# Kernel optimization log

Hardware: AMD Instinct MI355X
Metric: run time of the kernel (lower is better)

The kernel has to match this reference:

```python
import jax, jax.numpy as jnp
import numpy as np

B, S, E = 2, 4096, 2560
H, HKV, D = 8, 4, 256
WINDOW = 1024
SOFTCAP = 50.0
SCALING = 256.0 ** -0.5  # query_pre_attn_scalar = 256
EPS = 1e-6
MASK_VAL = -2.3819763e38


def rms_norm(x, w):
    # RMSNorm with add_unit_offset=True, computed in float32
    xf = x.astype(jnp.float32)
    out = xf * jax.lax.rsqrt(jnp.mean(xf * xf, axis=-1, keepdims=True) + EPS)
    return (out * (1.0 + w.astype(jnp.float32))).astype(x.dtype)


def apply_rotary_emb(x, cos, sin):
    # x: [B, S, h, D]; cos/sin: [S, D/2]; half-split rotation
    x1, x2 = jnp.split(x, 2, axis=-1)
    c = cos[None, :, None, :]
    s = sin[None, :, None, :]
    return jnp.concatenate([x1 * c - x2 * s, x2 * c + x1 * s], axis=-1)


def setup_inputs() -> dict:
    key = jax.random.key(0)
    ks = jax.random.split(key, 6)
    hidden_states = jax.random.normal(ks[0], (B, S, E), dtype=jnp.float32)
    # RoPE frequencies, theta=10000
    inv_freq = 1.0 / (10000.0 ** (np.arange(0, D, 2, dtype=np.float32) / D))
    t = np.arange(S, dtype=np.float32)
    freqs = np.outer(t, inv_freq)  # [S, D/2]
    freqs_cos = jnp.asarray(np.cos(freqs), dtype=jnp.float32)
    freqs_sin = jnp.asarray(np.sin(freqs), dtype=jnp.float32)
    kv_write_indices = jnp.arange(S, dtype=jnp.int32)
    k_cache = jnp.zeros((B, S, HKV, D), dtype=jnp.float32)
    v_cache = jnp.zeros((B, S, HKV, D), dtype=jnp.float32)
    # causal mask and causal+sliding-window mask (additive)
    i = np.arange(S)[:, None]
    j = np.arange(S)[None, :]
    causal = j <= i
    sliding = causal & ((i - j) < WINDOW)
    mask = jnp.asarray(np.where(causal, 0.0, MASK_VAL), dtype=jnp.float32)
    mask = jnp.broadcast_to(mask[None, None], (B, 1, S, S))
    local_mask = jnp.asarray(np.where(sliding, 0.0, MASK_VAL), dtype=jnp.float32)
    local_mask = jnp.broadcast_to(local_mask[None, None], (B, 1, S, S))
    w_qkv = jax.random.normal(ks[1], ((H + 2 * HKV) * D, E), dtype=jnp.float32) * (E ** -0.5)
    w_o = jax.random.normal(ks[2], (E, H * D), dtype=jnp.float32) * ((H * D) ** -0.5)
    q_norm_w = jnp.zeros((D,), dtype=jnp.float32)
    k_norm_w = jnp.zeros((D,), dtype=jnp.float32)
    return dict(hidden_states=hidden_states, freqs_cos=freqs_cos, freqs_sin=freqs_sin,
                kv_write_indices=kv_write_indices, k_cache=k_cache, v_cache=v_cache,
                mask=mask, local_mask=local_mask, w_qkv=w_qkv, w_o=w_o,
                q_norm_w=q_norm_w, k_norm_w=k_norm_w)


def reference(hidden_states, freqs_cos, freqs_sin, kv_write_indices, k_cache, v_cache,
              mask, local_mask, w_qkv, w_o, q_norm_w, k_norm_w):
    bsz, input_len, _ = hidden_states.shape
    qkv = jnp.einsum('bse,fe->bsf', hidden_states, w_qkv)
    xq, xk, xv = jnp.split(qkv, [H * D, H * D + HKV * D], axis=-1)
    xq = xq.reshape(bsz, input_len, H, D)
    xk = xk.reshape(bsz, input_len, HKV, D)
    xv = xv.reshape(bsz, input_len, HKV, D)
    # QK RMSNorm
    xq = rms_norm(xq, q_norm_w)
    xk = rms_norm(xk, k_norm_w)
    # RoPE
    xq = apply_rotary_emb(xq, freqs_cos, freqs_sin)
    xk = apply_rotary_emb(xk, freqs_cos, freqs_sin)
    # KV cache write
    k_cache = k_cache.at[:, kv_write_indices].set(xk)
    v_cache = v_cache.at[:, kv_write_indices].set(xv)
    kv_len = k_cache.shape[1]
    # GQA expand: [B, T, HKV, D] -> [B, T, H, D]
    nrep = H // HKV
    key = jnp.repeat(k_cache, nrep, axis=2)
    value = jnp.repeat(v_cache, nrep, axis=2)
    q = jnp.transpose(xq, (0, 2, 1, 3)) * SCALING   # [B, H, S, D]
    k = jnp.transpose(key, (0, 2, 1, 3))            # [B, H, T, D]
    v = jnp.transpose(value, (0, 2, 1, 3))
    scores = jnp.einsum('bhqd,bhkd->bhqk', q, k)
    # logit softcapping
    scores = jnp.tanh(scores / SOFTCAP) * SOFTCAP
    # attn_type == LOCAL_SLIDING -> use local (sliding-window) mask
    scores = scores + local_mask
    probs = jax.nn.softmax(scores.astype(jnp.float32), axis=-1).astype(q.dtype)
    out = jnp.einsum('bhqk,bhkd->bhqd', probs, v)
    out = jnp.transpose(out, (0, 2, 1, 3)).reshape(bsz, input_len, H * D)
    return jnp.einsum('bsf,ef->bse', out, w_o)
```

## Files before the change

### kernel.cpp

```cpp
#include <hip/hip_runtime.h>
#include <stdint.h>
#include <stddef.h>

#define B_    2
#define S_    4096
#define E_    2560
#define H_    8
#define HKV_  4
#define D_    256
#define F_    4096
#define HD_   2048
#define WIN_  1024
#define MASKNEG (-3.0e38f)

typedef __bf16 bf16;
typedef bf16  bf16x8 __attribute__((ext_vector_type(8)));
typedef bf16  bf16x4 __attribute__((ext_vector_type(4)));
typedef float f32x4  __attribute__((ext_vector_type(4)));
typedef uint32_t u32;

__device__ __forceinline__ void gl_lds16(const void* g, void* l) {
  __builtin_amdgcn_global_load_lds((const __attribute__((address_space(1))) void*)g,
                                   (__attribute__((address_space(3))) void*)l, 16, 0, 0);
}

__device__ __forceinline__ void bar_mf() {
  asm volatile("" ::: "memory");
  __builtin_amdgcn_s_barrier();
  asm volatile("" ::: "memory");
}

__device__ __forceinline__ float softcap50(float x) {
  float t = x * 0.02f;
  t = fminf(fmaxf(t, -15.f), 15.f);
  float e = __expf(2.f * t);
  return 50.f * ((e - 1.f) / (e + 1.f));
}

__device__ __forceinline__ u32 pkbf16(float a, float b) {
  union { bf16 h[2]; u32 u; } cv;
  cv.h[0] = (bf16)a; cv.h[1] = (bf16)b; return cv.u;
}

__global__ __launch_bounds__(256) void to_bf16_plain(const float* __restrict__ src,
                                                     bf16* __restrict__ dst, int n) {
  const int i = (blockIdx.x * 256 + threadIdx.x) * 8;
  if (i >= n) return;
  f32x4 a = *(const f32x4*)(src + i);
  f32x4 b = *(const f32x4*)(src + i + 4);
  bf16x8 o;
#pragma unroll
  for (int j = 0; j < 4; ++j) { o[j] = (bf16)a[j]; o[j + 4] = (bf16)b[j]; }
  *(bf16x8*)(dst + i) = o;
}

template <int EPI>
__global__ __launch_bounds__(512, 2) void gemm_8ph(
    const bf16* __restrict__ A, const bf16* __restrict__ Bw, int Kd, int NT,
    bf16* __restrict__ qo, bf16* __restrict__ ko, bf16* __restrict__ vto,
    float* __restrict__ C, int Nout, int row_base) {
  __shared__ bf16 Lds[2][4][128 * 64];

  const int tid  = threadIdx.x;
  const int lane = tid & 63;
  const int wave = tid >> 6;
  const int wm   = wave >> 2;
  const int wn   = wave & 3;
  const int l16  = lane & 15;
  const int quad = lane >> 4;

  const int nwg  = gridDim.x * gridDim.y;
  const int obid = blockIdx.y * gridDim.x + blockIdx.x;
  const int bid  = (obid & 7) * (nwg >> 3) + (obid >> 3);
  const int mt   = bid / gridDim.x;
  const int ntl  = bid - mt * gridDim.x;
  const int row0 = mt * 256, col0 = ntl * 256;

  const bf16* Ah[2] = {A  + (size_t)row0 * Kd, A  + (size_t)(row0 + 128) * Kd};
  const bf16* Bh[2] = {Bw + (size_t)col0 * Kd, Bw + (size_t)(col0 + 128) * Kd};

  auto stage = [&](int dbf, int hf, const bf16* src, int k0) {
#pragma unroll
    for (int i = 0; i < 2; ++i) {
      const int g = tid + i * 512;
      const int r = g >> 3, c = g & 7;
      gl_lds16(src + (size_t)r * Kd + k0 + ((c ^ (r & 7)) << 3),
               &Lds[dbf][hf][0] + g * 8);
    }
  };
  auto rdA = [&](int dbf, int i, int ks) -> bf16x8 {
    const int r = i * 16 + l16;
    return *(const bf16x8*)&Lds[dbf][wm][r * 64 + (((ks * 4 + quad) ^ (r & 7)) << 3)];
  };
  auto rdB = [&](int dbf, int j, int ks) -> bf16x8 {
    const int r = (wn & 1) * 64 + j * 16 + l16;
    return *(const bf16x8*)&Lds[dbf][2 + (wn >> 1)][r * 64 + (((ks * 4 + quad) ^ (r & 7)) << 3)];
  };

  f32x4 acc[8][4] = {};

  stage(0, 0, Ah[0], 0); stage(0, 1, Ah[1], 0);
  stage(0, 2, Bh[0], 0); stage(0, 3, Bh[1], 0);
  if (NT > 1) { stage(1, 2, Bh[0], 64); stage(1, 3, Bh[1], 64); }
  asm volatile("s_waitcnt vmcnt(4)" ::: "memory");
  bar_mf();

  int db = 0;
  for (int t = 0; t < NT; ++t, db ^= 1) {
    const int k1 = (t + 1) * 64, k2 = (t + 2) * 64;
    const bool st1 = (t + 1 < NT), st2 = (t + 2 < NT);

    bf16x8 bfr[4][2], a[4][2], a2[4][2];
#pragma unroll
    for (int j = 0; j < 4; ++j) { bfr[j][0] = rdB(db, j, 0); bfr[j][1] = rdB(db, j, 1); }
#pragma unroll
    for (int i = 0; i < 4; ++i) { a[i][0] = rdA(db, i, 0); a[i][1] = rdA(db, i, 1); }
    if (st1) stage(db ^ 1, 0, Ah[0], k1);
    bar_mf();
    __builtin_amdgcn_s_setprio(1);
#pragma unroll
    for (int i = 0; i < 2; ++i)
#pragma unroll
      for (int j = 0; j < 4; ++j) {
        acc[i][j] = __builtin_amdgcn_mfma_f32_16x16x32_bf16(a[i][0], bfr[j][0], acc[i][j], 0, 0, 0);
        acc[i][j] = __builtin_amdgcn_mfma_f32_16x16x32_bf16(a[i][1], bfr[j][1], acc[i][j], 0, 0, 0);
      }
    __builtin_amdgcn_s_setprio(0);
    bar_mf();

#pragma unroll
    for (int i = 0; i < 4; ++i) { a2[i][0] = rdA(db, i + 4, 0); a2[i][1] = rdA(db, i + 4, 1); }
    if (st1) stage(db ^ 1, 1, Ah[1], k1);
    bar_mf();
    __builtin_amdgcn_s_setprio(1);
#pragma unroll
    for (int i = 2; i < 4; ++i)
#pragma unroll
      for (int j = 0; j < 4; ++j) {
        acc[i][j] = __builtin_amdgcn_mfma_f32_16x16x32_bf16(a[i][0], bfr[j][0], acc[i][j], 0, 0, 0);
        acc[i][j] = __builtin_amdgcn_mfma_f32_16x16x32_bf16(a[i][1], bfr[j][1], acc[i][j], 0, 0, 0);
      }
    __builtin_amdgcn_s_setprio(0);
    bar_mf();

    if (st2) stage(db, 2, Bh[0], k2);
    bar_mf();
    __builtin_amdgcn_s_setprio(1);
#pragma unroll
    for (int i = 0; i < 2; ++i)
#pragma unroll
      for (int j = 0; j < 4; ++j) {
        acc[i + 4][j] = __builtin_amdgcn_mfma_f32_16x16x32_bf16(a2[i][0], bfr[j][0], acc[i + 4][j], 0, 0, 0);
        acc[i + 4][j] = __builtin_amdgcn_mfma_f32_16x16x32_bf16(a2[i][1], bfr[j][1], acc[i + 4][j], 0, 0, 0);
      }
    __builtin_amdgcn_s_setprio(0);
    bar_mf();

    if (st2) stage(db, 3, Bh[1], k2);
    bar_mf();
    __builtin_amdgcn_s_setprio(1);
#pragma unroll
    for (int i = 2; i < 4; ++i)
#pragma unroll
      for (int j = 0; j < 4; ++j) {
        acc[i + 4][j] = __builtin_amdgcn_mfma_f32_16x16x32_bf16(a2[i][0], bfr[j][0], acc[i + 4][j], 0, 0, 0);
        acc[i + 4][j] = __builtin_amdgcn_mfma_f32_16x16x32_bf16(a2[i][1], bfr[j][1], acc[i + 4][j], 0, 0, 0);
      }
    __builtin_amdgcn_s_setprio(0);
    if (st2) asm volatile("s_waitcnt vmcnt(4)" ::: "memory");
    else     asm volatile("s_waitcnt vmcnt(0)" ::: "memory");
    bar_mf();
  }

#pragma unroll
  for (int i = 0; i < 8; ++i) {
    const int rbase = row_base + row0 + wm * 128 + i * 16 + quad * 4;
#pragma unroll
    for (int j = 0; j < 4; ++j) {
      const int c = col0 + wn * 64 + j * 16 + l16;
      if constexpr (EPI == 1) {
        int head = c >> 8;
        const int d = c & 255;
        if (head < 12) {
          bf16* base; int nh;
          if (head < 8) { base = qo; nh = H_; }
          else          { base = ko; nh = HKV_; head -= 8; }
#pragma unroll
          for (int rr = 0; rr < 4; ++rr) {
            const int row = rbase + rr;
            const int bb = row >> 12, s = row & 4095;
            base[(((size_t)(bb * nh + head) * S_) + s) * D_ + d] = (bf16)acc[i][j][rr];
          }
        } else {
          const int kh = head - 12;
          const int bb = rbase >> 12, s0 = rbase & 4095;
          bf16x4 pk;
#pragma unroll
          for (int rr = 0; rr < 4; ++rr) pk[rr] = (bf16)acc[i][j][rr];
          *(bf16x4*)(vto + (((size_t)(bb * HKV_ + kh) * D_ + d) * S_ + s0)) = pk;
        }
      } else {
#pragma unroll
        for (int rr = 0; rr < 4; ++rr)
          C[(size_t)(rbase + rr) * Nout + c] = acc[i][j][rr];
      }
    }
  }
}

__global__ __launch_bounds__(192) void normrope2(
    bf16* __restrict__ q, bf16* __restrict__ k,
    const float* __restrict__ fcos, const float* __restrict__ fsin,
    const int* __restrict__ widx,
    const float* __restrict__ qnw, const float* __restrict__ knw) {
  const int bx  = blockIdx.x;
  const int b   = bx >> 12;
  const int s   = bx & 4095;
  const int tid = threadIdx.x;
  const int hh  = tid >> 4;
  const int g   = tid & 15;
  const int d0  = g * 16;

  const bool isq = (hh < 8);
  bf16* rowp = isq ? (q + (((size_t)(b * H_ + hh) * S_ + s) * D_ + d0))
                   : (k + (((size_t)(b * HKV_ + (hh - 8)) * S_ + s) * D_ + d0));
  float x[16];
  {
    bf16x8 v0 = *(const bf16x8*)rowp;
    bf16x8 v1 = *(const bf16x8*)(rowp + 8);
#pragma unroll
    for (int i = 0; i < 8; ++i) { x[i] = (float)v0[i]; x[i + 8] = (float)v1[i]; }
  }

  float ssq = 0.f;
#pragma unroll
  for (int i = 0; i < 16; ++i) ssq += x[i] * x[i];
#pragma unroll
  for (int off = 1; off < 16; off <<= 1) ssq += __shfl_xor(ssq, off);
  const float sc = rsqrtf(ssq * (1.0f / 256.0f) + 1e-6f);
  const float* w = isq ? qnw : knw;
#pragma unroll
  for (int i = 0; i < 16; ++i) x[i] = x[i] * sc * (1.0f + w[d0 + i]);

  const int fbase = (g < 8) ? d0 : (d0 - 128);
  const float* cp = fcos + (size_t)s * 128 + fbase;
  const float* sp = fsin + (size_t)s * 128 + fbase;
#pragma unroll
  for (int i = 0; i < 16; ++i) {
    const float c = cp[i], sn = sp[i];
    const float other = __shfl_xor(x[i], 8);
    x[i] = (g < 8) ? (x[i] * c - other * sn)
                   : (x[i] * c + other * sn);
  }
  if (isq) {
#pragma unroll
    for (int i = 0; i < 16; ++i) x[i] *= 0.0625f;
  }

  bf16x8 o0, o1;
#pragma unroll
  for (int i = 0; i < 8; ++i) { o0[i] = (bf16)x[i]; o1[i] = (bf16)x[i + 8]; }

  bf16* dstp = isq ? rowp
                   : (k + (((size_t)(b * HKV_ + (hh - 8)) * S_ + widx[s]) * D_ + d0));
  *(bf16x8*)dstp = o0;
  *(bf16x8*)(dstp + 8) = o1;
}

__global__ __launch_bounds__(256) void attn_mfma(const bf16* __restrict__ Q,
                                                 const bf16* __restrict__ K,
                                                 const bf16* __restrict__ Vt,
                                                 bf16* __restrict__ out) {
  __shared__ bf16 Ks[2][32 * 256];
  __shared__ bf16 Vs[2][256 * 32];

  const int hw  = blockIdx.x;
  const int lid = (hw & 7) * 128 + (hw >> 3);
  const int bx  = lid & 63;
  const int bh  = lid >> 6;
  const int b   = bh >> 3, h = bh & 7, kh = h >> 1;

  const int lane = threadIdx.x & 63;
  const int wave = threadIdx.x >> 6;
  const int l16  = lane & 15;
  const int qd   = lane >> 4;
  const int swz  = l16 & 7;

  const int q0w = bx * 64 + wave * 16;
  const int iq  = q0w + l16;

  const bf16* Kb = K  + ((size_t)(b * HKV_ + kh) * S_) * D_;
  const bf16* Vb = Vt + ((size_t)(b * HKV_ + kh) * D_) * S_;

  bf16x8 qf[8];
  {
    const bf16* qp = Q + (((size_t)(b * H_ + h) * S_ + iq) * D_) + qd * 8;
#pragma unroll
    for (int kc = 0; kc < 8; ++kc) qf[kc] = *(const bf16x8*)(qp + kc * 32);
  }

  f32x4 Od[16] = {};
  float m = MASKNEG, l = 0.f;

  int lo = bx * 64 - (WIN_ - 1); if (lo < 0) lo = 0;
  lo &= ~31;
  const int t1 = bx * 64 + 32;

  auto stage = [&](int buf, int kt) {
#pragma unroll
    for (int i = 0; i < 4; ++i) {
      const int r0  = wave * 8 + i * 2;
      const int row = r0 + (lane >> 5);
      const int c   = lane & 31;
      gl_lds16(Kb + (size_t)(kt + row) * D_ + ((c ^ (row & 7)) * 8),
               &Ks[buf][r0 * 256] + lane * 8);
    }
#pragma unroll
    for (int i = 0; i < 4; ++i) {
      const int d0 = (wave * 4 + i) * 16;
      const int d  = d0 + (lane >> 2);
      gl_lds16(Vb + (size_t)d * S_ + kt + (lane & 3) * 8,
               &Vs[buf][d0 * 32] + lane * 8);
    }
  };

  stage(0, lo);
  int buf = 0;

  for (int kt = lo; kt <= t1; kt += 32) {
    const bool pre = (kt + 32 <= t1);
    if (pre) {
      stage(buf ^ 1, kt + 32);
      asm volatile("s_waitcnt vmcnt(8)" ::: "memory");
    } else {
      asm volatile("s_waitcnt vmcnt(0)" ::: "memory");
    }
    __builtin_amdgcn_s_barrier();
    asm volatile("" ::: "memory");

    const bool dead = (kt > q0w + 15) || (kt + 31 < q0w - (WIN_ - 1));
    if (!dead) {
      f32x4 sacc[2] = {};
#pragma unroll
      for (int kc = 0; kc < 8; ++kc) {
        const int ch = ((kc * 4 + qd) ^ swz) * 8;
        bf16x8 k0 = *(const bf16x8*)&Ks[buf][l16 * 256 + ch];
        bf16x8 k1 = *(const bf16x8*)&Ks[buf][(l16 + 16) * 256 + ch];
        sacc[0] = __builtin_amdgcn_mfma_f32_16x16x32_bf16(k0, qf[kc], sacc[0], 0, 0, 0);
        sacc[1] = __builtin_amdgcn_mfma_f32_16x16x32_bf16(k1, qf[kc], sacc[1], 0, 0, 0);
      }

      float scv[8];
#pragma unroll
      for (int t = 0; t < 2; ++t)
#pragma unroll
        for (int r = 0; r < 4; ++r) {
          const int jj = kt + t * 16 + qd * 4 + r;
          const float a = softcap50(sacc[t][r]);
          scv[t * 4 + r] = (jj <= iq && (iq - jj) < WIN_) ? a : MASKNEG;
        }

      float mx = scv[0];
#pragma unroll
      for (int i = 1; i < 8; ++i) mx = fmaxf(mx, scv[i]);
      mx = fmaxf(mx, __shfl_xor(mx, 16));
      mx = fmaxf(mx, __shfl_xor(mx, 32));
      const float mn = fmaxf(m, mx);
      const float alpha = __expf(m - mn);

      float p[8], ls = 0.f;
#pragma unroll
      for (int i = 0; i < 8; ++i) {
        p[i] = (scv[i] > -1e37f) ? __expf(scv[i] - mn) : 0.f;
        ls += p[i];
      }
      ls += __shfl_xor(ls, 16);
      ls += __shfl_xor(ls, 32);
      l = l * alpha + ls;
      m = mn;
#pragma unroll
      for (int dt = 0; dt < 16; ++dt) Od[dt] *= alpha;

      const u32 w0 = pkbf16(p[0], p[1]);
      const u32 w1 = pkbf16(p[2], p[3]);
      const u32 w2 = pkbf16(p[4], p[5]);
      const u32 w3 = pkbf16(p[6], p[7]);
      const int sA = l16 + ((2 * qd) & 3) * 16;
      const int sB = l16 + ((2 * qd + 1) & 3) * 16;
      const int a0 = __shfl((int)w0, sA), a1 = __shfl((int)w1, sA);
      const int a2 = __shfl((int)w2, sA), a3 = __shfl((int)w3, sA);
      const int b0 = __shfl((int)w0, sB), b1 = __shfl((int)w1, sB);
      const int b2 = __shfl((int)w2, sB), b3 = __shfl((int)w3, sB);
      const bool thi = (qd >> 1) != 0;
      union { int i4[4]; bf16x8 v; } pf;
      pf.i4[0] = thi ? a2 : a0;
      pf.i4[1] = thi ? a3 : a1;
      pf.i4[2] = thi ? b2 : b0;
      pf.i4[3] = thi ? b3 : b1;

#pragma unroll
      for (int dt = 0; dt < 16; ++dt) {
        bf16x8 vf = *(const bf16x8*)&Vs[buf][(dt * 16 + l16) * 32 + qd * 8];
        Od[dt] = __builtin_amdgcn_mfma_f32_16x16x32_bf16(vf, pf.v, Od[dt], 0, 0, 0);
      }
    }

    asm volatile("" ::: "memory");
    __builtin_amdgcn_s_barrier();
    buf ^= 1;
  }

  const float inv = 1.f / l;
  bf16* op = out + ((size_t)b * S_ + iq) * HD_ + h * D_ + qd * 4;
#pragma unroll
  for (int dt = 0; dt < 16; ++dt) {
    bf16x4 o4;
#pragma unroll
    for (int r = 0; r < 4; ++r) o4[r] = (bf16)(Od[dt][r] * inv);
    *(bf16x4*)(op + dt * 16) = o4;
  }
}

extern "C" void kernel_launch(void* const* d_in, const int* in_sizes, int n_in,
                              void* d_out, int out_size, void* d_ws, size_t ws_size,
                              hipStream_t stream) {
  const float* hidden = (const float*)d_in[0];
  const float* fcos   = (const float*)d_in[1];
  const float* fsin   = (const float*)d_in[2];
  const int*   widx   = (const int*)d_in[3];
  const float* wqkv   = (const float*)d_in[8];
  const float* wo     = (const float*)d_in[9];
  const float* qnw    = (const float*)d_in[10];
  const float* knw    = (const float*)d_in[11];
  float* out = (float*)d_out;

  char* ws = (char*)d_ws;
  const size_t MB = 1024 * 1024;
  const bool big = ws_size >= 126 * MB;

  bf16* wb_bf = (bf16*)(ws);
  bf16* hb_bf = (bf16*)(ws + 20 * MB);
  bf16* q_ws  = (bf16*)(ws + (big ? 60 : 32) * MB);
  bf16* k_ws  = (bf16*)(ws + (big ? 92 : 64) * MB);
  bf16* vt_ws = (bf16*)(ws + (big ? 108 : 80) * MB);
  bf16* att_o = (bf16*)(ws);
  bf16* wo_bf = (bf16*)(ws + 32 * MB);

  to_bf16_plain<<<(F_ * E_ / 8 + 255) / 256, 256, 0, stream>>>(wqkv, wb_bf, F_ * E_);

  const int nch   = big ? 1 : 4;
  const int chrow = (B_ * S_) / nch;
  for (int c = 0; c < nch; ++c) {
    const int row_base = c * chrow;
    to_bf16_plain<<<(chrow * E_ / 8 + 255) / 256, 256, 0, stream>>>(
        hidden + (size_t)row_base * E_, hb_bf, chrow * E_);
    gemm_8ph<1><<<dim3(F_ / 256, chrow / 256), 512, 0, stream>>>(
        hb_bf, wb_bf, E_, E_ / 64, q_ws, k_ws, vt_ws, nullptr, 0, row_base);
  }

  normrope2<<<dim3(B_ * S_), 192, 0, stream>>>(q_ws, k_ws, fcos, fsin, widx, qnw, knw);
  attn_mfma<<<dim3(1024), 256, 0, stream>>>(q_ws, k_ws, vt_ws, att_o);
  to_bf16_plain<<<(E_ * HD_ / 8 + 255) / 256, 256, 0, stream>>>(wo, wo_bf, E_ * HD_);
  gemm_8ph<0><<<dim3(E_ / 256, (B_ * S_) / 256), 512, 0, stream>>>(
      att_o, wo_bf, HD_, HD_ / 64, nullptr, nullptr, nullptr, out, E_, 0);
  (void)in_sizes; (void)n_in; (void)out_size;
}
```

Baseline: 858.3 us.

## Drop online-softmax max tracking using softcap bound, permute K rows, narrower GEMM tiles

The attention kernel drops running-max tracking and rescaling. Softcapped scores are bounded by 50, so exp(score-50) is computed directly through a sigmoid-style exp2 formulation, with masking skipped on interior tiles. K rows are permuted at load time so the P fragment can be packed without cross-lane shuffles. GEMMs gain a BN template parameter: the output projection and the small-workspace QKV path use 128-wide N tiles to put more workgroups on the grid. This relies on the softcap bound for numerical safety and adds a templated tile path.

```diff
diff --git a/kernel.cpp b/kernel.cpp
--- a/kernel.cpp
+++ b/kernel.cpp
@@ -11,7 +11,6 @@
 #define F_    4096
 #define HD_   2048
 #define WIN_  1024
-#define MASKNEG (-3.0e38f)
 
 typedef __bf16 bf16;
 typedef bf16  bf16x8 __attribute__((ext_vector_type(8)));
@@ -28,13 +27,6 @@
   asm volatile("" ::: "memory");
   __builtin_amdgcn_s_barrier();
   asm volatile("" ::: "memory");
-}
-
-__device__ __forceinline__ float softcap50(float x) {
-  float t = x * 0.02f;
-  t = fminf(fmaxf(t, -15.f), 15.f);
-  float e = __expf(2.f * t);
-  return 50.f * ((e - 1.f) / (e + 1.f));
 }
 
 __device__ __forceinline__ u32 pkbf16(float a, float b) {
@@ -54,12 +46,14 @@
   *(bf16x8*)(dst + i) = o;
 }
 
-template <int EPI>
+template <int EPI, int BN>
 __global__ __launch_bounds__(512, 2) void gemm_8ph(
     const bf16* __restrict__ A, const bf16* __restrict__ Bw, int Kd, int NT,
     bf16* __restrict__ qo, bf16* __restrict__ ko, bf16* __restrict__ vto,
     float* __restrict__ C, int Nout, int row_base) {
-  __shared__ bf16 Lds[2][4][128 * 64];
+  constexpr int NBH = BN / 128;
+  constexpr int JT  = BN / 64;
+  __shared__ bf16 Lds[2][2 + NBH][128 * 64];
 
   const int tid  = threadIdx.x;
   const int lane = tid & 63;
@@ -74,10 +68,11 @@
   const int bid  = (obid & 7) * (nwg >> 3) + (obid >> 3);
   const int mt   = bid / gridDim.x;
   const int ntl  = bid - mt * gridDim.x;
-  const int row0 = mt * 256, col0 = ntl * 256;
-
-  const bf16* Ah[2] = {A  + (size_t)row0 * Kd, A  + (size_t)(row0 + 128) * Kd};
-  const bf16* Bh[2] = {Bw + (size_t)col0 * Kd, Bw + (size_t)(col0 + 128) * Kd};
+  const int row0 = mt * 256, col0 = ntl * BN;
+
+  const bf16* Ah[2] = {A + (size_t)row0 * Kd, A + (size_t)(row0 + 128) * Kd};
+  const bf16* Bh[2] = {Bw + (size_t)col0 * Kd,
+                       Bw + (size_t)(col0 + (NBH == 2 ? 128 : 0)) * Kd};
 
   auto stage = [&](int dbf, int hf, const bf16* src, int k0) {
 #pragma unroll
@@ -93,16 +88,22 @@
     return *(const bf16x8*)&Lds[dbf][wm][r * 64 + (((ks * 4 + quad) ^ (r & 7)) << 3)];
   };
   auto rdB = [&](int dbf, int j, int ks) -> bf16x8 {
-    const int r = (wn & 1) * 64 + j * 16 + l16;
-    return *(const bf16x8*)&Lds[dbf][2 + (wn >> 1)][r * 64 + (((ks * 4 + quad) ^ (r & 7)) << 3)];
+    const int colt = wn * (BN / 4) + j * 16 + l16;
+    const int r = colt & 127;
+    return *(const bf16x8*)&Lds[dbf][2 + (colt >> 7)][r * 64 + (((ks * 4 + quad) ^ (r & 7)) << 3)];
   };
 
-  f32x4 acc[8][4] = {};
+  f32x4 acc[8][JT] = {};
 
   stage(0, 0, Ah[0], 0); stage(0, 1, Ah[1], 0);
-  stage(0, 2, Bh[0], 0); stage(0, 3, Bh[1], 0);
-  if (NT > 1) { stage(1, 2, Bh[0], 64); stage(1, 3, Bh[1], 64); }
-  asm volatile("s_waitcnt vmcnt(4)" ::: "memory");
+#pragma unroll
+  for (int h = 0; h < NBH; ++h) stage(0, 2 + h, Bh[h], 0);
+  if (NT > 1) {
+#pragma unroll
+    for (int h = 0; h < NBH; ++h) stage(1, 2 + h, Bh[h], 64);
+  }
+  if constexpr (NBH == 2) asm volatile("s_waitcnt vmcnt(4)" ::: "memory");
+  else                    asm volatile("s_waitcnt vmcnt(2)" ::: "memory");
   bar_mf();
 
   int db = 0;
@@ -110,9 +111,9 @@
     const int k1 = (t + 1) * 64, k2 = (t + 2) * 64;
     const bool st1 = (t + 1 < NT), st2 = (t + 2 < NT);
 
-    bf16x8 bfr[4][2], a[4][2], a2[4][2];
-#pragma unroll
-    for (int j = 0; j < 4; ++j) { bfr[j][0] = rdB(db, j, 0); bfr[j][1] = rdB(db, j, 1); }
+    bf16x8 bfr[JT][2], a[4][2], a2[4][2];
+#pragma unroll
+    for (int j = 0; j < JT; ++j) { bfr[j][0] = rdB(db, j, 0); bfr[j][1] = rdB(db, j, 1); }
 #pragma unroll
     for (int i = 0; i < 4; ++i) { a[i][0] = rdA(db, i, 0); a[i][1] = rdA(db, i, 1); }
     if (st1) stage(db ^ 1, 0, Ah[0], k1);
@@ -121,7 +122,7 @@
 #pragma unroll
     for (int i = 0; i < 2; ++i)
 #pragma unroll
-      for (int j = 0; j < 4; ++j) {
+      for (int j = 0; j < JT; ++j) {
         acc[i][j] = __builtin_amdgcn_mfma_f32_16x16x32_bf16(a[i][0], bfr[j][0], acc[i][j], 0, 0, 0);
         acc[i][j] = __builtin_amdgcn_mfma_f32_16x16x32_bf16(a[i][1], bfr[j][1], acc[i][j], 0, 0, 0);
       }
@@ -136,7 +137,7 @@
 #pragma unroll
     for (int i = 2; i < 4; ++i)
 #pragma unroll
-      for (int j = 0; j < 4; ++j) {
+      for (int j = 0; j < JT; ++j) {
         acc[i][j] = __builtin_amdgcn_mfma_f32_16x16x32_bf16(a[i][0], bfr[j][0], acc[i][j], 0, 0, 0);
         acc[i][j] = __builtin_amdgcn_mfma_f32_16x16x32_bf16(a[i][1], bfr[j][1], acc[i][j], 0, 0, 0);
       }
@@ -149,26 +150,30 @@
 #pragma unroll
     for (int i = 0; i < 2; ++i)
 #pragma unroll
-      for (int j = 0; j < 4; ++j) {
+      for (int j = 0; j < JT; ++j) {
         acc[i + 4][j] = __builtin_amdgcn_mfma_f32_16x16x32_bf16(a2[i][0], bfr[j][0], acc[i + 4][j], 0, 0, 0);
         acc[i + 4][j] = __builtin_amdgcn_mfma_f32_16x16x32_bf16(a2[i][1], bfr[j][1], acc[i + 4][j], 0, 0, 0);
       }
     __builtin_amdgcn_s_setprio(0);
     bar_mf();
 
-    if (st2) stage(db, 3, Bh[1], k2);
+    if constexpr (NBH == 2) { if (st2) stage(db, 3, Bh[1], k2); }
     bar_mf();
     __builtin_amdgcn_s_setprio(1);
 #pragma unroll
     for (int i = 2; i < 4; ++i)
 #pragma unroll
-      for (int j = 0; j < 4; ++j) {
+      for (int j = 0; j < JT; ++j) {
         acc[i + 4][j] = __builtin_amdgcn_mfma_f32_16x16x32_bf16(a2[i][0], bfr[j][0], acc[i + 4][j], 0, 0, 0);
         acc[i + 4][j] = __builtin_amdgcn_mfma_f32_16x16x32_bf16(a2[i][1], bfr[j][1], acc[i + 4][j], 0, 0, 0);
       }
     __builtin_amdgcn_s_setprio(0);
-    if (st2) asm volatile("s_waitcnt vmcnt(4)" ::: "memory");
-    else     asm volatile("s_waitcnt vmcnt(0)" ::: "memory");
+    if (st2) {
+      if constexpr (NBH == 2) asm volatile("s_waitcnt vmcnt(4)" ::: "memory");
+      else                    asm volatile("s_waitcnt vmcnt(2)" ::: "memory");
+    } else {
+      asm volatile("s_waitcnt vmcnt(0)" ::: "memory");
+    }
     bar_mf();
   }
 
@@ -176,8 +181,8 @@
   for (int i = 0; i < 8; ++i) {
     const int rbase = row_base + row0 + wm * 128 + i * 16 + quad * 4;
 #pragma unroll
-    for (int j = 0; j < 4; ++j) {
-      const int c = col0 + wn * 64 + j * 16 + l16;
+    for (int j = 0; j < JT; ++j) {
+      const int c = col0 + wn * (BN / 4) + j * 16 + l16;
       if constexpr (EPI == 1) {
         int head = c >> 8;
         const int d = c & 255;
@@ -300,7 +305,7 @@
   }
 
   f32x4 Od[16] = {};
-  float m = MASKNEG, l = 0.f;
+  float lsum = 0.f;
 
   int lo = bx * 64 - (WIN_ - 1); if (lo < 0) lo = 0;
   lo &= ~31;
@@ -312,7 +317,8 @@
       const int r0  = wave * 8 + i * 2;
       const int row = r0 + (lane >> 5);
       const int c   = lane & 31;
-      gl_lds16(Kb + (size_t)(kt + row) * D_ + ((c ^ (row & 7)) * 8),
+      const int pk = (((row >> 2) & 3) << 3) + ((row >> 4) << 2) + (row & 3);
+      gl_lds16(Kb + (size_t)(kt + pk) * D_ + ((c ^ (row & 7)) * 8),
                &Ks[buf][r0 * 256] + lane * 8);
     }
 #pragma unroll
@@ -326,6 +332,9 @@
 
   stage(0, lo);
   int buf = 0;
+
+  const float c1 = 0.05770780163555853f;
+  const float c2 = -144.26950408889634f;
 
   for (int kt = lo; kt <= t1; kt += 32) {
     const bool pre = (kt + 32 <= t1);
@@ -350,53 +359,29 @@
         sacc[1] = __builtin_amdgcn_mfma_f32_16x16x32_bf16(k1, qf[kc], sacc[1], 0, 0, 0);
       }
 
-      float scv[8];
+      const bool interior = (kt + 31 <= q0w) && (kt >= q0w - 1008);
+      const int  kb0 = kt + qd * 8;
+      float p[8];
 #pragma unroll
       for (int t = 0; t < 2; ++t)
 #pragma unroll
         for (int r = 0; r < 4; ++r) {
-          const int jj = kt + t * 16 + qd * 4 + r;
-          const float a = softcap50(sacc[t][r]);
-          scv[t * 4 + r] = (jj <= iq && (iq - jj) < WIN_) ? a : MASKNEG;
+          const float x = sacc[t][r];
+          const float wv = __builtin_amdgcn_rcpf(exp2f(x * c1) + 1.0f);
+          float pp = exp2f(c2 * wv);
+          if (!interior) {
+            const int key = kb0 + t * 4 + r;
+            pp = (key <= iq && (iq - key) < WIN_) ? pp : 0.f;
+          }
+          p[t * 4 + r] = pp;
+          lsum += pp;
         }
 
-      float mx = scv[0];
-#pragma unroll
-      for (int i = 1; i < 8; ++i) mx = fmaxf(mx, scv[i]);
-      mx = fmaxf(mx, __shfl_xor(mx, 16));
-      mx = fmaxf(mx, __shfl_xor(mx, 32));
-      const float mn = fmaxf(m, mx);
-      const float alpha = __expf(m - mn);
-
-      float p[8], ls = 0.f;
-#pragma unroll
-      for (int i = 0; i < 8; ++i) {
-        p[i] = (scv[i] > -1e37f) ? __expf(scv[i] - mn) : 0.f;
-        ls += p[i];
-      }
-      ls += __shfl_xor(ls, 16);
-      ls += __shfl_xor(ls, 32);
-      l = l * alpha + ls;
-      m = mn;
-#pragma unroll
-      for (int dt = 0; dt < 16; ++dt) Od[dt] *= alpha;
-
-      const u32 w0 = pkbf16(p[0], p[1]);
-      const u32 w1 = pkbf16(p[2], p[3]);
-      const u32 w2 = pkbf16(p[4], p[5]);
-      const u32 w3 = pkbf16(p[6], p[7]);
-      const int sA = l16 + ((2 * qd) & 3) * 16;
-      const int sB = l16 + ((2 * qd + 1) & 3) * 16;
-      const int a0 = __shfl((int)w0, sA), a1 = __shfl((int)w1, sA);
-      const int a2 = __shfl((int)w2, sA), a3 = __shfl((int)w3, sA);
-      const int b0 = __shfl((int)w0, sB), b1 = __shfl((int)w1, sB);
-      const int b2 = __shfl((int)w2, sB), b3 = __shfl((int)w3, sB);
-      const bool thi = (qd >> 1) != 0;
-      union { int i4[4]; bf16x8 v; } pf;
-      pf.i4[0] = thi ? a2 : a0;
-      pf.i4[1] = thi ? a3 : a1;
-      pf.i4[2] = thi ? b2 : b0;
-      pf.i4[3] = thi ? b3 : b1;
+      union { u32 u[4]; bf16x8 v; } pf;
+      pf.u[0] = pkbf16(p[0], p[1]);
+      pf.u[1] = pkbf16(p[2], p[3]);
+      pf.u[2] = pkbf16(p[4], p[5]);
+      pf.u[3] = pkbf16(p[6], p[7]);
 
 #pragma unroll
       for (int dt = 0; dt < 16; ++dt) {
@@ -410,6 +395,8 @@
     buf ^= 1;
   }
 
+  float l = lsum + __shfl_xor(lsum, 16);
+  l += __shfl_xor(l, 32);
   const float inv = 1.f / l;
   bf16* op = out + ((size_t)b * S_ + iq) * HD_ + h * D_ + qd * 4;
 #pragma unroll
@@ -454,14 +441,18 @@
     const int row_base = c * chrow;
     to_bf16_plain<<<(chrow * E_ / 8 + 255) / 256, 256, 0, stream>>>(
         hidden + (size_t)row_base * E_, hb_bf, chrow * E_);
-    gemm_8ph<1><<<dim3(F_ / 256, chrow / 256), 512, 0, stream>>>(
-        hb_bf, wb_bf, E_, E_ / 64, q_ws, k_ws, vt_ws, nullptr, 0, row_base);
+    if (big)
+      gemm_8ph<1, 256><<<dim3(F_ / 256, chrow / 256), 512, 0, stream>>>(
+          hb_bf, wb_bf, E_, E_ / 64, q_ws, k_ws, vt_ws, nullptr, 0, row_base);
+    else
+      gemm_8ph<1, 128><<<dim3(F_ / 128, chrow / 256), 512, 0, stream>>>(
+          hb_bf, wb_bf, E_, E_ / 64, q_ws, k_ws, vt_ws, nullptr, 0, row_base);
   }
 
   normrope2<<<dim3(B_ * S_), 192, 0, stream>>>(q_ws, k_ws, fcos, fsin, widx, qnw, knw);
   attn_mfma<<<dim3(1024), 256, 0, stream>>>(q_ws, k_ws, vt_ws, att_o);
   to_bf16_plain<<<(E_ * HD_ / 8 + 255) / 256, 256, 0, stream>>>(wo, wo_bf, E_ * HD_);
-  gemm_8ph<0><<<dim3(E_ / 256, (B_ * S_) / 256), 512, 0, stream>>>(
+  gemm_8ph<0, 128><<<dim3(E_ / 128, (B_ * S_) / 256), 512, 0, stream>>>(
       att_o, wo_bf, HD_, HD_ / 64, nullptr, nullptr, nullptr, out, E_, 0);
   (void)in_sizes; (void)n_in; (void)out_size;
 }
```

Result: faster. 809.9 us (-5.6%).
